# Kernel tuning notes

Hardware: AMD Instinct MI355X
Metric: run time of the kernel (lower is better)

## Reference

```python
import jax, jax.numpy as jnp
import numpy as np

SCORE_THRESH = 0.05
NMS_THRESH = 0.5
DETS_PER_IMG = 100
IMG_W, IMG_H = 1333.0, 800.0
BBOX_XFORM_CLIP = float(np.log(1000.0 / 16.0))
WX, WY, WW, WH = 10.0, 10.0, 5.0, 5.0


def decode_boxes(rel, ref):
    widths = ref[:, 2] - ref[:, 0] + 1.0
    heights = ref[:, 3] - ref[:, 1] + 1.0
    ctr_x = ref[:, 0] + 0.5 * widths
    ctr_y = ref[:, 1] + 0.5 * heights
    dx = rel[:, 0] / WX
    dy = rel[:, 1] / WY
    dw = jnp.minimum(rel[:, 2] / WW, BBOX_XFORM_CLIP)
    dh = jnp.minimum(rel[:, 3] / WH, BBOX_XFORM_CLIP)
    pcx = dx * widths + ctr_x
    pcy = dy * heights + ctr_y
    pw = jnp.exp(dw) * widths
    ph = jnp.exp(dh) * heights
    return jnp.stack([pcx - 0.5 * pw, pcy - 0.5 * ph,
                      pcx + 0.5 * pw - 1.0, pcy + 0.5 * ph - 1.0], axis=1)


def pairwise_iou(b):
    # torchvision-style IoU (no +1), b: [n,4] xyxy
    area = (b[:, 2] - b[:, 0]) * (b[:, 3] - b[:, 1])
    lt = jnp.maximum(b[:, None, :2], b[None, :, :2])
    rb = jnp.minimum(b[:, None, 2:], b[None, :, 2:])
    wh = jnp.clip(rb - lt, 0.0)
    inter = wh[..., 0] * wh[..., 1]
    return inter / (area[:, None] + area[None, :] - inter + 1e-12)


def nms_keep(boxes, scores, valid):
    # masked greedy NMS; returns boolean keep mask in original order
    n = boxes.shape[0]
    order = jnp.argsort(-jnp.where(valid, scores, -jnp.inf))
    b = boxes[order]
    v = valid[order]
    iou = pairwise_iou(b)  # [n,n]
    idx = jnp.arange(n)

    def body(i, keep):
        suppressed = jnp.any(keep & (iou[i] > NMS_THRESH) & (idx < i))
        return keep.at[i].set(v[i] & ~suppressed)

    keep_sorted = jax.lax.fori_loop(0, n, body, jnp.zeros(n, dtype=bool))
    return jnp.zeros(n, dtype=bool).at[order].set(keep_sorted)


def setup_inputs() -> dict:
    key = jax.random.key(0)
    k1, k2, k3, k4, k5 = jax.random.split(key, 5)
    C, K = 16, 2048
    class_logit = jax.random.normal(k1, (C * K, 2), jnp.float32)
    box_regression = jax.random.normal(k2, (C * K, 8), jnp.float32) * 0.5
    x1 = jax.random.uniform(k3, (K,)) * (IMG_W - 220.0)
    y1 = jax.random.uniform(k4, (K,)) * (IMG_H - 220.0)
    wh = 20.0 + jax.random.uniform(k5, (K, 2)) * 180.0
    proposal_boxes = jnp.stack([x1, y1, x1 + wh[:, 0], y1 + wh[:, 1]], axis=1).astype(jnp.float32)
    unique_labels = jnp.arange(1, C + 1, dtype=jnp.int32)
    return {"class_logit": class_logit, "box_regression": box_regression,
            "proposal_boxes": proposal_boxes, "unique_labels": unique_labels}


def reference(class_logit, box_regression, proposal_boxes, unique_labels):
    C = unique_labels.shape[0]
    K = proposal_boxes.shape[0]
    # softmax over binary logits, take foreground prob
    prob = jax.nn.softmax(class_logit, axis=1)[:, 1]  # [C*K]
    rel = box_regression[:, 4:8]
    ref_boxes = jnp.tile(proposal_boxes, (C, 1))  # class-major [C*K,4]
    dec = decode_boxes(rel, ref_boxes)
    # clip_to_image (remove_empty=False), TO_REMOVE = 1
    dec = jnp.stack([jnp.clip(dec[:, 0], 0.0, IMG_W - 1.0),
                     jnp.clip(dec[:, 1], 0.0, IMG_H - 1.0),
                     jnp.clip(dec[:, 2], 0.0, IMG_W - 1.0),
                     jnp.clip(dec[:, 3], 0.0, IMG_H - 1.0)], axis=1)
    boxes_c = dec.reshape(C, K, 4)
    scores_c = prob.reshape(C, K)
    valid = scores_c > SCORE_THRESH
    keep = jax.vmap(nms_keep)(boxes_c, scores_c, valid).reshape(-1)  # [C*K]
    flat_scores = scores_c.reshape(-1)
    n_det = jnp.sum(keep)
    masked = jnp.where(keep, flat_scores, -jnp.inf)
    kth = jax.lax.top_k(masked, DETS_PER_IMG)[0][-1]  # 100th largest kept score
    keep_final = jnp.where(n_det > DETS_PER_IMG, keep & (flat_scores >= kth), keep)
    labels = jnp.broadcast_to(unique_labels[:, None], (C, K)).reshape(-1)
    out_boxes = jnp.where(keep_final[:, None], dec, 0.0)
    out_scores = jnp.where(keep_final, flat_scores, 0.0)
    out5 = jnp.concatenate([out_boxes, out_scores[:, None]], axis=1)  # [C*K,5]
    return out5, labels, keep_final
```

## Files before the change

kernel.cpp:

```cpp
#include <hip/hip_runtime.h>
#include <hip/hip_bf16.h>

#define NCLS 16
#define NBOX 2048
#define NTOT (NCLS * NBOX)
#define NCHUNK 32
#define SCORE_THRESH 0.05f
#define NMS_THRESH 0.5f
#define DETS_PER_IMG 100
#define TOPC 128
#define BBOX_CLIP 4.135166556742356f

typedef unsigned long long u64;

__device__ __forceinline__ u64 sel_mx(u64 a, u64 b, bool keepmax) {
    u64 mx = (a > b) ? a : b;
    u64 mn = (a > b) ? b : a;
    return keepmax ? mx : mn;
}

__global__ __launch_bounds__(1024) void sortmask_kernel(
    const float* __restrict__ logits,
    const float* __restrict__ regr,
    const float* __restrict__ props,
    float4* __restrict__ dec,
    u64* __restrict__ keys_out,
    u64* __restrict__ maskT)
{
    int blk = blockIdx.x;
    int c = blk >> 4;
    int p = blk & 15;
    int tid = threadIdx.x;

    int w = tid >> 6, l = tid & 63;
    int p0 = w * 128 + l;
    int p1 = p0 + 64;
    __shared__ float4 decv[NBOX];
    __shared__ float4 boxu[NBOX];
    u64* runs = (u64*)boxu;
    float4* box = boxu;

    u64 e01[2];
#pragma unroll
    for (int s = 0; s < 2; s++) {
#pragma clang fp contract(off)
        int t = s ? p1 : p0;
        int i = c * NBOX + t;
        float x0 = logits[2 * i + 0];
        float x1 = logits[2 * i + 1];
        float m = fmaxf(x0, x1);
        float e0f = expf(x0 - m);
        float e1f = expf(x1 - m);
        float score = e1f / (e0f + e1f);

        float px1 = props[4 * t + 0];
        float py1 = props[4 * t + 1];
        float px2 = props[4 * t + 2];
        float py2 = props[4 * t + 3];

        float bw = px2 - px1 + 1.0f;
        float bh = py2 - py1 + 1.0f;
        float cx = px1 + 0.5f * bw;
        float cy = py1 + 0.5f * bh;

        float dx = regr[8 * i + 4] / 10.0f;
        float dy = regr[8 * i + 5] / 10.0f;
        float dw = fminf(regr[8 * i + 6] / 5.0f, BBOX_CLIP);
        float dh = fminf(regr[8 * i + 7] / 5.0f, BBOX_CLIP);

        float pcx = dx * bw + cx;
        float pcy = dy * bh + cy;
        float pw  = expf(dw) * bw;
        float ph  = expf(dh) * bh;

        float b0 = pcx - 0.5f * pw;
        float b1 = pcy - 0.5f * ph;
        float b2 = pcx + 0.5f * pw - 1.0f;
        float b3 = pcy + 0.5f * ph - 1.0f;

        b0 = fminf(fmaxf(b0, 0.0f), 1332.0f);
        b1 = fminf(fmaxf(b1, 0.0f), 799.0f);
        b2 = fminf(fmaxf(b2, 0.0f), 1332.0f);
        b3 = fminf(fmaxf(b3, 0.0f), 799.0f);

        float4 bb = make_float4(b0, b1, b2, b3);
        decv[t] = bb;
        if (p == 0) dec[i] = bb;

        unsigned mono = 0u;
        if (score > SCORE_THRESH) mono = __float_as_uint(score) | 0x80000000u;
        e01[s] = ((u64)mono << 32) | (u64)(unsigned)(NBOX - 1 - t);
    }
    u64 e0 = e01[0], e1 = e01[1];

#pragma unroll
    for (int k = 2; k <= 128; k <<= 1) {
        bool d0 = ((l & k) == 0);
        bool d1 = (((l + 64) & k) == 0);
#pragma unroll
        for (int j = k >> 1; j > 0; j >>= 1) {
            if (j == 64) {
                u64 mx = (e0 > e1) ? e0 : e1;
                u64 mn = (e0 > e1) ? e1 : e0;
                e0 = d0 ? mx : mn;
                e1 = d0 ? mn : mx;
            } else {
                u64 q0 = __shfl_xor(e0, j);
                u64 q1 = __shfl_xor(e1, j);
                bool hi = (l & j) != 0;
                e0 = sel_mx(e0, q0, d0 ^ hi);
                e1 = sel_mx(e1, q1, d1 ^ hi);
            }
        }
    }

    runs[w * 128 + l] = e0;
    runs[w * 128 + 64 + l] = e1;
    __syncthreads();

    int rank0 = 0, rank1 = 0;
#pragma unroll
    for (int R = 0; R < 16; R++) {
        const u64* run = runs + R * 128;
        int pa = 0, pb = 0;
#pragma unroll
        for (int step = 128; step >= 1; step >>= 1) {
            int qa = pa + step - 1;
            int qb = pb + step - 1;
            u64 va = run[qa & 127];
            u64 vb = run[qb & 127];
            if (qa < 128 && va > e0) pa += step;
            if (qb < 128 && vb > e1) pb += step;
        }
        rank0 += pa;
        rank1 += pb;
    }

    int i0 = (NBOX - 1) - (int)(e0 & 0xFFFFFFFFull);
    int i1 = (NBOX - 1) - (int)(e1 & 0xFFFFFFFFull);
    float4 g0 = decv[i0];
    float4 g1 = decv[i1];
    if (p == 0) {
        keys_out[c * NBOX + rank0] = e0;
        keys_out[c * NBOX + rank1] = e1;
    }
    __syncthreads();
    box[rank0] = g0;
    box[rank1] = g1;
    __syncthreads();

    int r = tid & 63;
    int g = tid >> 6;

    for (int pass = 0; pass < 2; pass++) {
#pragma clang fp contract(off)
        int Jc = pass ? (31 - p) : p;
        int j = Jc * 64 + r;
        float4 jb = box[j];
        float jar = (jb.z - jb.x) * (jb.w - jb.y);
        float hj = 0.5f * jar;
        float colC = hj + 5e-13f;

        for (int I = g; I <= Jc; I += 16) {
            u64 wm = 0;
            int rbase = I * 64;
#pragma unroll
            for (int i2 = 0; i2 < 64; i2++) {
#pragma clang fp contract(off)
                int gi = rbase + i2;
                float4 rb = box[gi];
                float ar = (rb.z - rb.x) * (rb.w - rb.y);
                float rha = 0.5f * ar;
                float lx = fmaxf(rb.x, jb.x);
                float ly = fmaxf(rb.y, jb.y);
                float rx = fminf(rb.z, jb.z);
                float ry = fminf(rb.w, jb.w);
                float ww = fmaxf(rx - lx, 0.0f);
                float hh = fmaxf(ry - ly, 0.0f);
                float inter = ww * hh;
                float s  = rha + colC;
                float band = 2e-6f * s;
                float delta = fmaf(1.5f, inter, -s);
                bool over = delta > band;
                bool amb = fabsf(delta) <= band;
                if (__any(amb)) {
                    float un = ar + jar - inter + 1e-12f;
                    float iou = inter / un;
                    bool ovx = iou > NMS_THRESH;
                    over = amb ? ovx : over;
                }
                if (over) wm |= 1ull << i2;
            }
            if (I == Jc) wm &= (1ull << r) - 1ull;
            maskT[((size_t)c * NCHUNK + I) * NBOX + j] = wm;
        }
    }
}

__global__ __launch_bounds__(64) void resolve_kernel(
    const u64* __restrict__ keys,
    const u64* __restrict__ maskT,
    unsigned* __restrict__ keepbits,
    unsigned* __restrict__ compact,
    int* __restrict__ nkept)
{
    int c = blockIdx.x;
    int l = threadIdx.x;
    const u64* MT = maskT + (size_t)c * NCHUNK * NBOX;
    const u64* K  = keys + (size_t)c * NBOX;

    unsigned sup = 0;
    int offset = 0;
    u64 tm[2][NCHUNK - 1];

#pragma unroll
    for (int t = 0; t < NCHUNK - 1; t++)
        tm[0][t] = MT[(size_t)(1 + t) * 64 + l];
    u64 diag = MT[l];
    u64 key  = K[l];

#pragma unroll
    for (int I = 0; I < NCHUNK; I++) {
        u64 diagN = diag, keyN = key;
        if (I + 1 < NCHUNK) {
            const u64* rowpN = MT + (size_t)(I + 1) * NBOX + l;
#pragma unroll
            for (int t = 0; t < NCHUNK - 2 - I; t++)
                tm[(I + 1) & 1][t] = rowpN[(size_t)(I + 2 + t) * 64];
            diagN = MT[(size_t)(I + 1) * NBOX + (size_t)(I + 1) * 64 + l];
            keyN  = K[(I + 1) * 64 + l];
        }
        __builtin_amdgcn_sched_barrier(0);

        unsigned mono = (unsigned)(key >> 32);
        bool av = (mono != 0u) && (((sup >> I) & 1u) == 0u);
        u64 kept = 0;
        u64 availB = __ballot(av);
        while (availB) {
            u64 front = __ballot(av && ((diag & availB) == 0ull));
            kept |= front;
            bool fr = ((front >> l) & 1ull) != 0ull;
            bool sp = ((diag & front) != 0ull);
            av = av && !fr && !sp;
            availB = __ballot(av);
        }

        int idx = (NBOX - 1) - (int)(key & 0xFFFFFFFFull);
        bool isk = ((kept >> l) & 1ull) != 0ull;
        keepbits[c * NBOX + idx] = isk ? (mono & 0x7FFFFFFFu) : 0u;

        int pos = offset + __popcll(kept & ((1ull << l) - 1ull));
        if (isk && pos < TOPC) compact[c * TOPC + pos] = mono;
        offset += __popcll(kept);

#pragma unroll
        for (int t = 0; t < NCHUNK - 1 - I; t++)
            sup |= (tm[I & 1][t] & kept) ? (1u << (I + 1 + t)) : 0u;

        diag = diagN;
        key  = keyN;
    }

    for (int t = offset + l; t < TOPC; t += 64) compact[c * TOPC + t] = 0u;
    if (l == 0) nkept[c] = offset;
}

__global__ __launch_bounds__(256) void selectwrite_kernel(
    const unsigned* __restrict__ compact,
    const int* __restrict__ nkept,
    const unsigned* __restrict__ keepbits,
    const float4* __restrict__ dec,
    const int* __restrict__ ulabels,
    float* __restrict__ out)
{
    __shared__ unsigned ls[NCLS * TOPC];
    __shared__ int s_stats[2];
    int tid = threadIdx.x;

    for (int t = tid; t < NCLS * TOPC; t += 256) ls[t] = compact[t];
    __syncthreads();

    if (tid < 64) {
        int l = tid;
        int n_c = (l < NCLS) ? nkept[l] : 0;
        int nd = n_c;
#pragma unroll
        for (int off = 32; off > 0; off >>= 1) nd += __shfl_down(nd, off);
        nd = __shfl(nd, 0);

        unsigned kth = 0u;
        if (nd > DETS_PER_IMG) {
            const unsigned* my = &ls[(l & 15) * TOPC];
            bool active = (l < NCLS);
            unsigned prefix = 0u;
            for (int bit = 31; bit >= 0; bit--) {
                unsigned cand = prefix | (1u << bit);
                int cnt = 0;
                if (active) {
                    if (my[TOPC - 1] >= cand) cnt = TOPC;
                    else {
                        int pos = 0;
#pragma unroll
                        for (int step = 64; step >= 1; step >>= 1)
                            if (my[pos + step - 1] >= cand) pos += step;
                        cnt = pos;
                    }
                }
#pragma unroll
                for (int off = 32; off > 0; off >>= 1) cnt += __shfl_down(cnt, off);
                cnt = __shfl(cnt, 0);
                if (cnt >= DETS_PER_IMG) prefix = cand;
            }
            kth = prefix & 0x7FFFFFFFu;
        }
        if (l == 0) { s_stats[0] = nd; s_stats[1] = (int)kth; }
    }
    __syncthreads();

    int n_det = s_stats[0];
    unsigned kth = (unsigned)s_stats[1];

    int i = blockIdx.x * 256 + tid;
    unsigned kb = keepbits[i];
    bool kf = kb && (n_det <= DETS_PER_IMG || kb >= kth);

    float4 b = dec[i];
    float* o5 = out + (size_t)i * 5;
    if (kf) {
        o5[0] = b.x; o5[1] = b.y; o5[2] = b.z; o5[3] = b.w;
        o5[4] = __uint_as_float(kb);
    } else {
        o5[0] = 0.0f; o5[1] = 0.0f; o5[2] = 0.0f; o5[3] = 0.0f; o5[4] = 0.0f;
    }

    int c = i >> 11;
    out[NTOT * 5 + i] = (float)ulabels[c];
    out[NTOT * 5 + NTOT + i] = kf ? 1.0f : 0.0f;
}

extern "C" void kernel_launch(void* const* d_in, const int* in_sizes, int n_in,
                              void* d_out, int out_size, void* d_ws, size_t ws_size,
                              hipStream_t stream) {
    (void)in_sizes; (void)n_in; (void)out_size; (void)ws_size;

    const float* class_logit    = (const float*)d_in[0];
    const float* box_regression = (const float*)d_in[1];
    const float* proposal_boxes = (const float*)d_in[2];
    const int*   unique_labels  = (const int*)d_in[3];

    char* ws = (char*)d_ws;
    float4* dec        = (float4*)(ws + 0);
    u64* keys          = (u64*)(ws + 524288);
    u64* maskT         = (u64*)(ws + 786432);
    unsigned* keepbits = (unsigned*)(ws + 9175040);
    unsigned* compact  = (unsigned*)(ws + 9306112);
    int* nkept         = (int*)(ws + 9314304);

    float* out = (float*)d_out;

    sortmask_kernel<<<NCLS * 16, 1024, 0, stream>>>(class_logit, box_regression,
                                                    proposal_boxes, dec, keys,
                                                    maskT);
    resolve_kernel<<<NCLS, 64, 0, stream>>>(keys, maskT, keepbits,
                                            compact, nkept);
    selectwrite_kernel<<<NTOT / 256, 256, 0, stream>>>(compact, nkept, keepbits,
                                                       dec, unique_labels, out);
}
```

Before: 136.4 us.

## Split fused sort/mask kernel into sort-decode and separate IoU mask kernel

```diff
diff --git a/kernel.cpp b/kernel.cpp
--- a/kernel.cpp
+++ b/kernel.cpp
@@ -19,26 +19,23 @@
     return keepmax ? mx : mn;
 }
 
-__global__ __launch_bounds__(1024) void sortmask_kernel(
+__global__ __launch_bounds__(1024) void sortdecode_kernel(
     const float* __restrict__ logits,
     const float* __restrict__ regr,
     const float* __restrict__ props,
     float4* __restrict__ dec,
     u64* __restrict__ keys_out,
-    u64* __restrict__ maskT)
+    float4* __restrict__ sbox4)
 {
     int blk = blockIdx.x;
-    int c = blk >> 4;
-    int p = blk & 15;
+    int h = blk & 3;
+    int c = blk >> 2;
     int tid = threadIdx.x;
-
     int w = tid >> 6, l = tid & 63;
     int p0 = w * 128 + l;
     int p1 = p0 + 64;
     __shared__ float4 decv[NBOX];
-    __shared__ float4 boxu[NBOX];
-    u64* runs = (u64*)boxu;
-    float4* box = boxu;
+    __shared__ u64 runs[NBOX];
 
     u64 e01[2];
 #pragma unroll
@@ -85,7 +82,7 @@
 
         float4 bb = make_float4(b0, b1, b2, b3);
         decv[t] = bb;
-        if (p == 0) dec[i] = bb;
+        if (h == 0) dec[i] = bb;
 
         unsigned mono = 0u;
         if (score > SCORE_THRESH) mono = __float_as_uint(score) | 0x80000000u;
@@ -118,43 +115,58 @@
     runs[w * 128 + 64 + l] = e1;
     __syncthreads();
 
-    int rank0 = 0, rank1 = 0;
-#pragma unroll
-    for (int R = 0; R < 16; R++) {
-        const u64* run = runs + R * 128;
-        int pa = 0, pb = 0;
-#pragma unroll
-        for (int step = 128; step >= 1; step >>= 1) {
-            int qa = pa + step - 1;
-            int qb = pb + step - 1;
-            u64 va = run[qa & 127];
-            u64 vb = run[qb & 127];
-            if (qa < 128 && va > e0) pa += step;
-            if (qb < 128 && vb > e1) pb += step;
-        }
-        rank0 += pa;
-        rank1 += pb;
-    }
-
-    int i0 = (NBOX - 1) - (int)(e0 & 0xFFFFFFFFull);
-    int i1 = (NBOX - 1) - (int)(e1 & 0xFFFFFFFFull);
-    float4 g0 = decv[i0];
-    float4 g1 = decv[i1];
-    if (p == 0) {
+    if ((w >> 2) == h) {
+        int rank0 = 0, rank1 = 0;
+#pragma unroll
+        for (int R = 0; R < 16; R++) {
+            const u64* run = runs + R * 128;
+            int pa = 0, pb = 0;
+#pragma unroll
+            for (int step = 128; step >= 1; step >>= 1) {
+                int qa = pa + step - 1;
+                int qb = pb + step - 1;
+                u64 va = run[qa & 127];
+                u64 vb = run[qb & 127];
+                if (qa < 128 && va > e0) pa += step;
+                if (qb < 128 && vb > e1) pb += step;
+            }
+            rank0 += pa;
+            rank1 += pb;
+        }
+
+        int i0 = (NBOX - 1) - (int)(e0 & 0xFFFFFFFFull);
+        int i1 = (NBOX - 1) - (int)(e1 & 0xFFFFFFFFull);
+        float4 g0 = decv[i0];
+        float4 g1 = decv[i1];
         keys_out[c * NBOX + rank0] = e0;
         keys_out[c * NBOX + rank1] = e1;
-    }
-    __syncthreads();
-    box[rank0] = g0;
-    box[rank1] = g1;
+        sbox4[c * NBOX + rank0] = g0;
+        sbox4[c * NBOX + rank1] = g1;
+    }
+}
+
+__global__ __launch_bounds__(1024) void mask_kernel(
+    const float4* __restrict__ sbox4,
+    u64* __restrict__ maskT)
+{
+    int blk = blockIdx.x;
+    int v = blk >> 8;
+    int rem = blk & 255;
+    int c = rem >> 4;
+    int p = rem & 15;
+    int tid = threadIdx.x;
+    __shared__ float4 box[NBOX];
+
+    for (int i = tid; i < NBOX; i += 1024)
+        box[i] = sbox4[c * NBOX + i];
     __syncthreads();
 
     int r = tid & 63;
     int g = tid >> 6;
 
-    for (int pass = 0; pass < 2; pass++) {
+    {
 #pragma clang fp contract(off)
-        int Jc = pass ? (31 - p) : p;
+        int Jc = v ? (31 - p) : p;
         int j = Jc * 64 + r;
         float4 jb = box[j];
         float jar = (jb.z - jb.x) * (jb.w - jb.y);
@@ -351,16 +363,18 @@
     char* ws = (char*)d_ws;
     float4* dec        = (float4*)(ws + 0);
     u64* keys          = (u64*)(ws + 524288);
-    u64* maskT         = (u64*)(ws + 786432);
-    unsigned* keepbits = (unsigned*)(ws + 9175040);
-    unsigned* compact  = (unsigned*)(ws + 9306112);
-    int* nkept         = (int*)(ws + 9314304);
+    float4* sbox4      = (float4*)(ws + 786432);
+    u64* maskT         = (u64*)(ws + 1310720);
+    unsigned* keepbits = (unsigned*)(ws + 9699328);
+    unsigned* compact  = (unsigned*)(ws + 9830400);
+    int* nkept         = (int*)(ws + 9838592);
 
     float* out = (float*)d_out;
 
-    sortmask_kernel<<<NCLS * 16, 1024, 0, stream>>>(class_logit, box_regression,
-                                                    proposal_boxes, dec, keys,
-                                                    maskT);
+    sortdecode_kernel<<<NCLS * 4, 1024, 0, stream>>>(class_logit, box_regression,
+                                                     proposal_boxes, dec, keys,
+                                                     sbox4);
+    mask_kernel<<<512, 1024, 0, stream>>>(sbox4, maskT);
     resolve_kernel<<<NCLS, 64, 0, stream>>>(keys, maskT, keepbits,
                                             compact, nkept);
     selectwrite_kernel<<<NTOT / 256, 256, 0, stream>>>(compact, nkept, keepbits,
```

Result: slower. 142.2 us (+4.3%).

## Fuse resolve and select-write kernels using last-block atomic and spin flag

Applied to the files above, without the earlier changes.

```diff
diff --git a/kernel.cpp b/kernel.cpp
--- a/kernel.cpp
+++ b/kernel.cpp
@@ -25,12 +25,14 @@
     const float* __restrict__ props,
     float4* __restrict__ dec,
     u64* __restrict__ keys_out,
-    u64* __restrict__ maskT)
+    u64* __restrict__ maskT,
+    int* __restrict__ flags)
 {
     int blk = blockIdx.x;
     int c = blk >> 4;
     int p = blk & 15;
     int tid = threadIdx.x;
+    if (blk == 0 && tid == 0) { flags[0] = 0; flags[1] = 0; }
 
     int w = tid >> 6, l = tid & 63;
     int p0 = w * 128 + l;
@@ -197,17 +199,24 @@
     }
 }
 
-__global__ __launch_bounds__(64) void resolve_kernel(
+__global__ __launch_bounds__(64, 1) void resolvewrite_kernel(
     const u64* __restrict__ keys,
     const u64* __restrict__ maskT,
+    const float4* __restrict__ dec,
+    const int* __restrict__ ulabels,
     unsigned* __restrict__ keepbits,
     unsigned* __restrict__ compact,
-    int* __restrict__ nkept)
+    int* __restrict__ nkept,
+    int* __restrict__ stats,
+    int* __restrict__ flags,
+    float* __restrict__ out)
 {
     int c = blockIdx.x;
     int l = threadIdx.x;
     const u64* MT = maskT + (size_t)c * NCHUNK * NBOX;
     const u64* K  = keys + (size_t)c * NBOX;
+
+    __shared__ unsigned ls[NCLS * TOPC];
 
     unsigned sup = 0;
     int offset = 0;
@@ -263,26 +272,18 @@
 
     for (int t = offset + l; t < TOPC; t += 64) compact[c * TOPC + t] = 0u;
     if (l == 0) nkept[c] = offset;
-}
-
-__global__ __launch_bounds__(256) void selectwrite_kernel(
-    const unsigned* __restrict__ compact,
-    const int* __restrict__ nkept,
-    const unsigned* __restrict__ keepbits,
-    const float4* __restrict__ dec,
-    const int* __restrict__ ulabels,
-    float* __restrict__ out)
-{
-    __shared__ unsigned ls[NCLS * TOPC];
-    __shared__ int s_stats[2];
-    int tid = threadIdx.x;
-
-    for (int t = tid; t < NCLS * TOPC; t += 256) ls[t] = compact[t];
-    __syncthreads();
-
-    if (tid < 64) {
-        int l = tid;
+    __threadfence();
+
+    int got = 0;
+    if (l == 0) got = atomicAdd(&flags[0], 1);
+    got = __shfl(got, 0);
+
+    if (got == NCLS - 1) {
+        __threadfence();
+        for (int t = l; t < NCLS * TOPC; t += 64) ls[t] = compact[t];
         int n_c = (l < NCLS) ? nkept[l] : 0;
+        __syncthreads();
+
         int nd = n_c;
 #pragma unroll
         for (int off = 32; off > 0; off >>= 1) nd += __shfl_down(nd, off);
@@ -313,29 +314,40 @@
             }
             kth = prefix & 0x7FFFFFFFu;
         }
-        if (l == 0) { s_stats[0] = nd; s_stats[1] = (int)kth; }
+
+        if (l == 0) {
+            stats[0] = nd;
+            stats[1] = (int)kth;
+            __threadfence();
+            __hip_atomic_store(&flags[1], 1, __ATOMIC_RELEASE,
+                               __HIP_MEMORY_SCOPE_AGENT);
+        }
+    } else {
+        if (l == 0) {
+            while (__hip_atomic_load(&flags[1], __ATOMIC_ACQUIRE,
+                                     __HIP_MEMORY_SCOPE_AGENT) == 0) {}
+        }
     }
     __syncthreads();
 
-    int n_det = s_stats[0];
-    unsigned kth = (unsigned)s_stats[1];
-
-    int i = blockIdx.x * 256 + tid;
-    unsigned kb = keepbits[i];
-    bool kf = kb && (n_det <= DETS_PER_IMG || kb >= kth);
-
-    float4 b = dec[i];
-    float* o5 = out + (size_t)i * 5;
-    if (kf) {
-        o5[0] = b.x; o5[1] = b.y; o5[2] = b.z; o5[3] = b.w;
-        o5[4] = __uint_as_float(kb);
-    } else {
-        o5[0] = 0.0f; o5[1] = 0.0f; o5[2] = 0.0f; o5[3] = 0.0f; o5[4] = 0.0f;
-    }
-
-    int c = i >> 11;
-    out[NTOT * 5 + i] = (float)ulabels[c];
-    out[NTOT * 5 + NTOT + i] = kf ? 1.0f : 0.0f;
+    int n_det = stats[0];
+    unsigned kth = (unsigned)stats[1];
+    float lab = (float)ulabels[c];
+    for (int t = l; t < NBOX; t += 64) {
+        int i = c * NBOX + t;
+        unsigned kb = keepbits[i];
+        bool kf = kb && (n_det <= DETS_PER_IMG || kb >= kth);
+        float4 b = dec[i];
+        float* o5 = out + (size_t)i * 5;
+        if (kf) {
+            o5[0] = b.x; o5[1] = b.y; o5[2] = b.z; o5[3] = b.w;
+            o5[4] = __uint_as_float(kb);
+        } else {
+            o5[0] = 0.0f; o5[1] = 0.0f; o5[2] = 0.0f; o5[3] = 0.0f; o5[4] = 0.0f;
+        }
+        out[NTOT * 5 + i] = lab;
+        out[NTOT * 5 + NTOT + i] = kf ? 1.0f : 0.0f;
+    }
 }
 
 extern "C" void kernel_launch(void* const* d_in, const int* in_sizes, int n_in,
@@ -355,14 +367,15 @@
     unsigned* keepbits = (unsigned*)(ws + 9175040);
     unsigned* compact  = (unsigned*)(ws + 9306112);
     int* nkept         = (int*)(ws + 9314304);
+    int* stats         = (int*)(ws + 9314368);
+    int* flags         = (int*)(ws + 9314432);
 
     float* out = (float*)d_out;
 
     sortmask_kernel<<<NCLS * 16, 1024, 0, stream>>>(class_logit, box_regression,
                                                     proposal_boxes, dec, keys,
-                                                    maskT);
-    resolve_kernel<<<NCLS, 64, 0, stream>>>(keys, maskT, keepbits,
-                                            compact, nkept);
-    selectwrite_kernel<<<NTOT / 256, 256, 0, stream>>>(compact, nkept, keepbits,
-                                                       dec, unique_labels, out);
+                                                    maskT, flags);
+    resolvewrite_kernel<<<NCLS, 64, 0, stream>>>(keys, maskT, dec, unique_labels,
+                                                 keepbits, compact, nkept,
+                                                 stats, flags, out);
 }
```

After: 150.8 us. 10.6% more time.
